# Kernel optimization log

Hardware: AMD Instinct MI355X
Metric: run time of the kernel (lower is better)

## Reference

```python
import jax, jax.numpy as jnp
import numpy as np

H = 1024
L = 2

def setup_inputs() -> dict:
    key = jax.random.key(0)
    k1, k2, k3, k4, k5 = jax.random.split(key, 5)
    B, S = 32, 2048
    scale = 1.0 / np.sqrt(H)
    return {
        "query": jax.random.normal(k1, (B, 1, H * L), dtype=jnp.float32),
        "keys": jax.random.normal(k2, (B, S, H), dtype=jnp.float32),
        "Wa_w": jax.random.normal(k3, (H * L, H), dtype=jnp.float32) * scale,
        "Wa_b": jnp.zeros((H,), dtype=jnp.float32),
        "Ua_w": jax.random.normal(k4, (H, H), dtype=jnp.float32) * scale,
        "Ua_b": jnp.zeros((H,), dtype=jnp.float32),
        "Va_w": jax.random.normal(k5, (H, 1), dtype=jnp.float32) * scale,
        "Va_b": jnp.zeros((1,), dtype=jnp.float32),
    }

def reference(query, keys, Wa_w, Wa_b, Ua_w, Ua_b, Va_w, Va_b):
    # query: [B,1,H*L], keys: [B,S,H]
    q = jnp.einsum('bqd,dh->bqh', query, Wa_w) + Wa_b   # [B,1,H]
    k = jnp.einsum('bsd,dh->bsh', keys, Ua_w) + Ua_b    # [B,S,H]
    e = jnp.tanh(q + k)                                  # [B,S,H]
    scores = jnp.einsum('bsh,ho->bso', e, Va_w) + Va_b   # [B,S,1]
    scores = scores[:, :, 0][:, None, :]                 # [B,1,S]
    weights = jax.nn.softmax(scores, axis=-1)            # [B,1,S]
    context = jnp.einsum('bqs,bsh->bqh', weights, keys)  # [B,1,H]
    return (context, weights)
```

## Files before the change

kernel.cpp:

```cpp
#include <hip/hip_runtime.h>
#include <hip/hip_bf16.h>


typedef __attribute__((ext_vector_type(8))) short short8;
typedef __attribute__((ext_vector_type(4))) float floatx4;

typedef const __attribute__((address_space(1))) unsigned int gu32;
typedef __attribute__((address_space(3))) unsigned int lu32;

__device__ __forceinline__ unsigned short f2bf(float f) {
    union { float f; unsigned int u; } c; c.f = f;
    unsigned int u = c.u + 0x7fffu + ((c.u >> 16) & 1u);
    return (unsigned short)(u >> 16);
}

__device__ __forceinline__ unsigned int f2bf2(float lo, float hi) {
#if __has_builtin(__builtin_amdgcn_cvt_pk_bf16_f32)
    auto r = __builtin_amdgcn_cvt_pk_bf16_f32(lo, hi);
    unsigned int u; __builtin_memcpy(&u, &r, 4);
    return u;
#else
    return (unsigned int)f2bf(lo) | ((unsigned int)f2bf(hi) << 16);
#endif
}

__device__ __forceinline__ void gld16(const unsigned short* g, unsigned short* l) {
    __builtin_amdgcn_global_load_lds(
        (gu32*)(uintptr_t)g,
        (lu32*)(unsigned int)(uintptr_t)l,
        16, 0, 0);
}

__global__ __launch_bounds__(256) void qproj_k(
    const float* __restrict__ query, const float* __restrict__ Wa,
    const float* __restrict__ Wab, const float* __restrict__ Uab,
    float* __restrict__ qws)
{
    __shared__ float qs[2048];
    __shared__ float red[16*64];
    const int tid = threadIdx.x;
    const int b = blockIdx.x, hc = blockIdx.y;
    #pragma unroll
    for (int i = 0; i < 8; i++) qs[tid + 256*i] = query[b*2048 + tid + 256*i];
    __syncthreads();
    const int hq = tid & 15;
    const int dg = tid >> 4;
    const float4* wp = reinterpret_cast<const float4*>(Wa + (size_t)(dg*128)*1024 + hc*64 + hq*4);
    const float* qp = qs + dg*128;
    float4 a0; a0.x = a0.y = a0.z = a0.w = 0.f;
    float4 a1; a1.x = a1.y = a1.z = a1.w = 0.f;
    #pragma unroll 4
    for (int d = 0; d < 128; d += 2) {
        float q0 = qp[d], q1 = qp[d+1];
        float4 w0 = wp[(size_t)d*256];
        float4 w1 = wp[(size_t)(d+1)*256];
        a0.x += q0*w0.x; a0.y += q0*w0.y; a0.z += q0*w0.z; a0.w += q0*w0.w;
        a1.x += q1*w1.x; a1.y += q1*w1.y; a1.z += q1*w1.z; a1.w += q1*w1.w;
    }
    a0.x += a1.x; a0.y += a1.y; a0.z += a1.z; a0.w += a1.w;
    *reinterpret_cast<float4*>(red + dg*64 + hq*4) = a0;
    __syncthreads();
    if (tid < 64) {
        float v = 0.f;
        #pragma unroll
        for (int g = 0; g < 16; g++) v += red[g*64 + tid];
        int hh = hc*64 + tid;
        qws[b*1024 + hh] = v + Wab[hh] + Uab[hh];
    }
}

__global__ __launch_bounds__(256) void uat_k(const float* __restrict__ Ua,
                                             unsigned short* __restrict__ uat)
{
    __shared__ unsigned short t[64][65];
    const int x = threadIdx.x & 63, yy = threadIdx.x >> 6;
    const int d0 = blockIdx.x*64, h0 = blockIdx.y*64;
    #pragma unroll
    for (int i = 0; i < 16; i++) {
        int y = yy*16 + i;
        t[y][x] = f2bf(Ua[(size_t)(d0+y)*1024 + h0 + x]);
    }
    __syncthreads();
    #pragma unroll
    for (int i = 0; i < 16; i++) {
        int y = yy*16 + i;
        uat[(size_t)(h0+y)*1024 + d0 + x] = t[x][y];
    }
}

__global__ __launch_bounds__(256) void score_gemm_fast(
    const float* __restrict__ keys,
    const unsigned short* __restrict__ uat,
    const float* __restrict__ qws,
    const float* __restrict__ Va,
    float* __restrict__ partial)
{
    __shared__ unsigned short aS[2][128*32];
    __shared__ unsigned short bS[2][128*32];
    const int tid = threadIdx.x;
    const int b = blockIdx.z;
    const int s0 = blockIdx.x * 128;
    const int h0 = blockIdx.y * 128;
    const int lane = tid & 63, wave = tid >> 6;
    const int quad = lane >> 4, l15 = lane & 15;
    const int wm = (wave & 1) * 64, wn = (wave >> 1) * 64;

    const int srow = lane >> 2;
    const int schunk = (lane & 3) ^ ((srow >> 1) & 3);

    floatx4 acc[4][4];
    #pragma unroll
    for (int i = 0; i < 4; i++)
        #pragma unroll
        for (int j = 0; j < 4; j++) acc[i][j] = (floatx4)0.0f;

    const float* kA = keys + (size_t)(b*2048 + s0)*1024;
    const unsigned short* ubase = uat + (size_t)h0*1024;
    const int c0 = wave*2, c1 = wave*2 + 1;
    const size_t boff0 = (size_t)(c0*16 + srow)*1024 + schunk*8;
    const size_t boff1 = (size_t)(c1*16 + srow)*1024 + schunk*8;

    const int arow0 = tid >> 2, ac = tid & 3;

    gld16(ubase + boff0, bS[0] + c0*512);
    gld16(ubase + boff1, bS[0] + c1*512);
    #pragma unroll
    for (int i = 0; i < 2; i++) {
        int row = arow0 + 64*i;
        int sl  = ac ^ ((row >> 1) & 3);
        const float* gp = kA + (size_t)row*1024 + ac*8;
        float4 v0 = *reinterpret_cast<const float4*>(gp);
        float4 v1 = *reinterpret_cast<const float4*>(gp + 4);
        uint4 w;
        w.x = f2bf2(v0.x, v0.y); w.y = f2bf2(v0.z, v0.w);
        w.z = f2bf2(v1.x, v1.y); w.w = f2bf2(v1.z, v1.w);
        *reinterpret_cast<uint4*>(aS[0] + row*32 + sl*8) = w;
    }
    __syncthreads();

    int cur = 0;
    for (int kt = 0; kt < 31; ++kt) {
        const int nxt = cur ^ 1;
        const int k1 = (kt + 1) << 5;

        gld16(ubase + boff0 + k1, bS[nxt] + c0*512);
        gld16(ubase + boff1 + k1, bS[nxt] + c1*512);
        float4 pa0[2], pa1[2];
        #pragma unroll
        for (int i = 0; i < 2; i++) {
            int row = arow0 + 64*i;
            const float* gp = kA + (size_t)row*1024 + k1 + ac*8;
            pa0[i] = *reinterpret_cast<const float4*>(gp);
            pa1[i] = *reinterpret_cast<const float4*>(gp + 4);
        }

        short8 af[4], bf8[4];
        #pragma unroll
        for (int i = 0; i < 4; i++) {
            int row = wm + 16*i + l15;
            af[i] = *reinterpret_cast<const short8*>(aS[cur] + row*32 + ((quad ^ ((row>>1)&3)) * 8));
        }
        #pragma unroll
        for (int j = 0; j < 4; j++) {
            int row = wn + 16*j + l15;
            bf8[j] = *reinterpret_cast<const short8*>(bS[cur] + row*32 + ((quad ^ ((row>>1)&3)) * 8));
        }
        __builtin_amdgcn_s_setprio(1);
        #pragma unroll
        for (int i = 0; i < 4; i++)
            #pragma unroll
            for (int j = 0; j < 4; j++)
                acc[i][j] = __builtin_amdgcn_mfma_f32_16x16x32_bf16(af[i], bf8[j], acc[i][j], 0, 0, 0);
        __builtin_amdgcn_s_setprio(0);

        #pragma unroll
        for (int i = 0; i < 2; i++) {
            int row = arow0 + 64*i;
            int sl  = ac ^ ((row >> 1) & 3);
            uint4 w;
            w.x = f2bf2(pa0[i].x, pa0[i].y); w.y = f2bf2(pa0[i].z, pa0[i].w);
            w.z = f2bf2(pa1[i].x, pa1[i].y); w.w = f2bf2(pa1[i].z, pa1[i].w);
            *reinterpret_cast<uint4*>(aS[nxt] + row*32 + sl*8) = w;
        }
        __syncthreads();
        cur = nxt;
    }

    {
        short8 af[4], bf8[4];
        #pragma unroll
        for (int i = 0; i < 4; i++) {
            int row = wm + 16*i + l15;
            af[i] = *reinterpret_cast<const short8*>(aS[cur] + row*32 + ((quad ^ ((row>>1)&3)) * 8));
        }
        #pragma unroll
        for (int j = 0; j < 4; j++) {
            int row = wn + 16*j + l15;
            bf8[j] = *reinterpret_cast<const short8*>(bS[cur] + row*32 + ((quad ^ ((row>>1)&3)) * 8));
        }
        __builtin_amdgcn_s_setprio(1);
        #pragma unroll
        for (int i = 0; i < 4; i++)
            #pragma unroll
            for (int j = 0; j < 4; j++)
                acc[i][j] = __builtin_amdgcn_mfma_f32_16x16x32_bf16(af[i], bf8[j], acc[i][j], 0, 0, 0);
        __builtin_amdgcn_s_setprio(0);
    }

    float qv[4], vav[4];
    #pragma unroll
    for (int j = 0; j < 4; j++) {
        int n = h0 + wn + 16*j + l15;
        qv[j]  = qws[b*1024 + n];
        vav[j] = Va[n];
    }
    const int slot = blockIdx.y * 2 + (wave >> 1);
    #pragma unroll
    for (int i = 0; i < 4; i++) {
        #pragma unroll
        for (int r = 0; r < 4; r++) {
            float p = 0.f;
            #pragma unroll
            for (int j = 0; j < 4; j++) {
                float x = qv[j] + acc[i][j][r];
                float e = __expf(2.f * x);
                float t = 1.f - 2.f * __builtin_amdgcn_rcpf(e + 1.f);
                p += vav[j] * t;
            }
            #pragma unroll
            for (int off = 1; off < 16; off <<= 1) p += __shfl_xor(p, off, 64);
            if (l15 == 0) {
                int m = wm + 16*i + quad*4 + r;
                partial[((size_t)b*16 + slot)*2048 + s0 + m] = p;
            }
        }
    }
}

__global__ __launch_bounds__(256) void softmax_k(const float* __restrict__ partial,
                                                 float* __restrict__ out_w)
{
    const int tid = threadIdx.x;
    const int b = blockIdx.x;
    __shared__ float wred[4], wred2[4];
    float sc[8];
    float mx = -3.0e38f;
    #pragma unroll
    for (int i = 0; i < 8; i++) {
        int s = tid + 256*i;
        float v = 0.f;
        #pragma unroll
        for (int ht = 0; ht < 16; ht++) v += partial[((size_t)b*16 + ht)*2048 + s];
        sc[i] = v; mx = fmaxf(mx, v);
    }
    #pragma unroll
    for (int off = 32; off >= 1; off >>= 1) mx = fmaxf(mx, __shfl_xor(mx, off, 64));
    if ((tid & 63) == 0) wred[tid >> 6] = mx;
    __syncthreads();
    mx = fmaxf(fmaxf(wred[0], wred[1]), fmaxf(wred[2], wred[3]));
    float e[8]; float lsum = 0.f;
    #pragma unroll
    for (int i = 0; i < 8; i++) { e[i] = __expf(sc[i] - mx); lsum += e[i]; }
    #pragma unroll
    for (int off = 32; off >= 1; off >>= 1) lsum += __shfl_xor(lsum, off, 64);
    if ((tid & 63) == 0) wred2[tid >> 6] = lsum;
    __syncthreads();
    float inv = 1.0f / (wred2[0] + wred2[1] + wred2[2] + wred2[3]);
    #pragma unroll
    for (int i = 0; i < 8; i++) out_w[b*2048 + tid + 256*i] = e[i] * inv;
}

__global__ __launch_bounds__(256) void ctx_k(const float* __restrict__ keys,
                                             const float* __restrict__ w,
                                             float* __restrict__ ctxp, int sper)
{
    const int tid = threadIdx.x;
    const int b = blockIdx.x, sc = blockIdx.y;
    const float4* k4 = reinterpret_cast<const float4*>(keys) + (size_t)(b*2048 + sc*sper)*256;
    const float* wp = w + b*2048 + sc*sper;
    float4 a; a.x = a.y = a.z = a.w = 0.f;
    #pragma unroll 4
    for (int s = 0; s < sper; s++) {
        float wv = wp[s];
        float4 kv = k4[(size_t)s*256 + tid];
        a.x += wv*kv.x; a.y += wv*kv.y; a.z += wv*kv.z; a.w += wv*kv.w;
    }
    reinterpret_cast<float4*>(ctxp)[((size_t)b*gridDim.y + sc)*256 + tid] = a;
}

__global__ __launch_bounds__(256) void ctxsum_k(const float* __restrict__ ctxp,
                                                float* __restrict__ out, int nc)
{
    const int idx = blockIdx.x*256 + threadIdx.x;
    const int b = idx >> 10, h = idx & 1023;
    float v = 0.f;
    for (int s = 0; s < nc; s++) v += ctxp[((size_t)b*nc + s)*1024 + h];
    out[idx] = v;
}

extern "C" void kernel_launch(void* const* d_in, const int* in_sizes, int n_in,
                              void* d_out, int out_size, void* d_ws, size_t ws_size,
                              hipStream_t stream)
{
    const float* query = (const float*)d_in[0];
    const float* keys  = (const float*)d_in[1];
    const float* Wa_w  = (const float*)d_in[2];
    const float* Wa_b  = (const float*)d_in[3];
    const float* Ua_w  = (const float*)d_in[4];
    const float* Ua_b  = (const float*)d_in[5];
    const float* Va_w  = (const float*)d_in[6];

    char* ws = (char*)d_ws;
    float*          qws     = (float*)(ws);
    unsigned short* uat     = (unsigned short*)(ws + (131072));
    float*          partial = (float*)(ws + (131072 + 2097152));
    float*          ctxp    = (float*)(ws + (131072 + 2097152 + 4194304));

    float* out_ctx = (float*)d_out;
    float* out_w   = out_ctx + 32*1024;

    qproj_k        <<<dim3(32, 16),    256, 0, stream>>>(query, Wa_w, Wa_b, Ua_b, qws);
    uat_k          <<<dim3(16, 16),    256, 0, stream>>>(Ua_w, uat);
    score_gemm_fast<<<dim3(16, 8, 32), 256, 0, stream>>>(keys, uat, qws, Va_w, partial);
    softmax_k      <<<dim3(32),        256, 0, stream>>>(partial, out_w);
    ctx_k          <<<dim3(32, 16),    256, 0, stream>>>(keys, out_w, ctxp, 128);
    ctxsum_k       <<<dim3(128),       256, 0, stream>>>(ctxp, out_ctx, 16);
}
```

Measured before the change: 665.7 us.

## Pre-convert keys to swizzled bf16 buffer and load GEMM A-tiles directly to LDS

Result: slower. 725.5 us (+9.0%).

```diff
diff --git a/kernel.cpp b/kernel.cpp
--- a/kernel.cpp
+++ b/kernel.cpp
@@ -88,17 +88,44 @@
     }
 }
 
+__global__ __launch_bounds__(256) void kb16_k(const float* __restrict__ keys,
+                                              unsigned short* __restrict__ kb)
+{
+    const size_t t = (size_t)blockIdx.x*256 + threadIdx.x;
+    const size_t rg = t >> 5;
+    const int g = (int)(t & 31);
+    const int s = (int)(rg & 2047);
+    const int p = (s >> 1) & 3;
+    const float4* in4 = reinterpret_cast<const float4*>(keys + rg*1024 + g*32);
+    uint4* out4 = reinterpret_cast<uint4*>(kb + rg*1024 + g*32);
+    float4 v[8];
+    #pragma unroll
+    for (int q = 0; q < 8; q++) v[q] = in4[q];
+    #pragma unroll
+    for (int j = 0; j < 4; j++) {
+        int jc = j ^ p;
+        uint4 w;
+        w.x = f2bf2(v[2*jc].x,   v[2*jc].y);
+        w.y = f2bf2(v[2*jc].z,   v[2*jc].w);
+        w.z = f2bf2(v[2*jc+1].x, v[2*jc+1].y);
+        w.w = f2bf2(v[2*jc+1].z, v[2*jc+1].w);
+        out4[j] = w;
+    }
+}
+
 __global__ __launch_bounds__(256) void score_gemm_fast(
-    const float* __restrict__ keys,
+    const unsigned short* __restrict__ kb16,
     const unsigned short* __restrict__ uat,
     const float* __restrict__ qws,
     const float* __restrict__ Va,
-    float* __restrict__ partial)
+    float* __restrict__ partial,
+    int b0)
 {
     __shared__ unsigned short aS[2][128*32];
     __shared__ unsigned short bS[2][128*32];
     const int tid = threadIdx.x;
-    const int b = blockIdx.z;
+    const int bz = blockIdx.z;
+    const int b = b0 + bz;
     const int s0 = blockIdx.x * 128;
     const int h0 = blockIdx.y * 128;
     const int lane = tid & 63, wave = tid >> 6;
@@ -107,35 +134,25 @@
 
     const int srow = lane >> 2;
     const int schunk = (lane & 3) ^ ((srow >> 1) & 3);
-
-    floatx4 acc[4][4];
-    #pragma unroll
-    for (int i = 0; i < 4; i++)
-        #pragma unroll
-        for (int j = 0; j < 4; j++) acc[i][j] = (floatx4)0.0f;
-
-    const float* kA = keys + (size_t)(b*2048 + s0)*1024;
+    const int c0 = wave*2, c1 = wave*2 + 1;
     const unsigned short* ubase = uat + (size_t)h0*1024;
-    const int c0 = wave*2, c1 = wave*2 + 1;
     const size_t boff0 = (size_t)(c0*16 + srow)*1024 + schunk*8;
     const size_t boff1 = (size_t)(c1*16 + srow)*1024 + schunk*8;
 
-    const int arow0 = tid >> 2, ac = tid & 3;
-
+    const unsigned short* kA = kb16 + (size_t)(bz*2048 + s0)*1024;
+    const size_t aoff0 = (size_t)(tid >> 2)*1024 + (size_t)(tid & 3)*8;
+    const size_t aoff1 = (size_t)(64 + (tid >> 2))*1024 + (size_t)(tid & 3)*8;
+
+    floatx4 acc[4][4];
+    #pragma unroll
+    for (int i = 0; i < 4; i++)
+        #pragma unroll
+        for (int j = 0; j < 4; j++) acc[i][j] = (floatx4)0.0f;
+
+    gld16(kA + aoff0,    aS[0] + wave*512);
+    gld16(kA + aoff1,    aS[0] + 2048 + wave*512);
     gld16(ubase + boff0, bS[0] + c0*512);
     gld16(ubase + boff1, bS[0] + c1*512);
-    #pragma unroll
-    for (int i = 0; i < 2; i++) {
-        int row = arow0 + 64*i;
-        int sl  = ac ^ ((row >> 1) & 3);
-        const float* gp = kA + (size_t)row*1024 + ac*8;
-        float4 v0 = *reinterpret_cast<const float4*>(gp);
-        float4 v1 = *reinterpret_cast<const float4*>(gp + 4);
-        uint4 w;
-        w.x = f2bf2(v0.x, v0.y); w.y = f2bf2(v0.z, v0.w);
-        w.z = f2bf2(v1.x, v1.y); w.w = f2bf2(v1.z, v1.w);
-        *reinterpret_cast<uint4*>(aS[0] + row*32 + sl*8) = w;
-    }
     __syncthreads();
 
     int cur = 0;
@@ -143,16 +160,10 @@
         const int nxt = cur ^ 1;
         const int k1 = (kt + 1) << 5;
 
+        gld16(kA + aoff0 + k1,    aS[nxt] + wave*512);
+        gld16(kA + aoff1 + k1,    aS[nxt] + 2048 + wave*512);
         gld16(ubase + boff0 + k1, bS[nxt] + c0*512);
         gld16(ubase + boff1 + k1, bS[nxt] + c1*512);
-        float4 pa0[2], pa1[2];
-        #pragma unroll
-        for (int i = 0; i < 2; i++) {
-            int row = arow0 + 64*i;
-            const float* gp = kA + (size_t)row*1024 + k1 + ac*8;
-            pa0[i] = *reinterpret_cast<const float4*>(gp);
-            pa1[i] = *reinterpret_cast<const float4*>(gp + 4);
-        }
 
         short8 af[4], bf8[4];
         #pragma unroll
@@ -165,23 +176,12 @@
             int row = wn + 16*j + l15;
             bf8[j] = *reinterpret_cast<const short8*>(bS[cur] + row*32 + ((quad ^ ((row>>1)&3)) * 8));
         }
-        __builtin_amdgcn_s_setprio(1);
         #pragma unroll
         for (int i = 0; i < 4; i++)
             #pragma unroll
             for (int j = 0; j < 4; j++)
                 acc[i][j] = __builtin_amdgcn_mfma_f32_16x16x32_bf16(af[i], bf8[j], acc[i][j], 0, 0, 0);
-        __builtin_amdgcn_s_setprio(0);
-
-        #pragma unroll
-        for (int i = 0; i < 2; i++) {
-            int row = arow0 + 64*i;
-            int sl  = ac ^ ((row >> 1) & 3);
-            uint4 w;
-            w.x = f2bf2(pa0[i].x, pa0[i].y); w.y = f2bf2(pa0[i].z, pa0[i].w);
-            w.z = f2bf2(pa1[i].x, pa1[i].y); w.w = f2bf2(pa1[i].z, pa1[i].w);
-            *reinterpret_cast<uint4*>(aS[nxt] + row*32 + sl*8) = w;
-        }
+
         __syncthreads();
         cur = nxt;
     }
@@ -198,13 +198,11 @@
             int row = wn + 16*j + l15;
             bf8[j] = *reinterpret_cast<const short8*>(bS[cur] + row*32 + ((quad ^ ((row>>1)&3)) * 8));
         }
-        __builtin_amdgcn_s_setprio(1);
         #pragma unroll
         for (int i = 0; i < 4; i++)
             #pragma unroll
             for (int j = 0; j < 4; j++)
                 acc[i][j] = __builtin_amdgcn_mfma_f32_16x16x32_bf16(af[i], bf8[j], acc[i][j], 0, 0, 0);
-        __builtin_amdgcn_s_setprio(0);
     }
 
     float qv[4], vav[4];
@@ -315,14 +313,23 @@
     unsigned short* uat     = (unsigned short*)(ws + (131072));
     float*          partial = (float*)(ws + (131072 + 2097152));
     float*          ctxp    = (float*)(ws + (131072 + 2097152 + 4194304));
+    const size_t BASE = 131072 + 2097152 + 4194304 + 2097152;
+    unsigned short* kb16 = (unsigned short*)(ws + BASE);
+
+    size_t avail = (ws_size > BASE) ? (ws_size - BASE) : 0;
+    int nb = 32;
+    while (nb > 1 && (size_t)nb * 2048 * 1024 * 2 > avail) nb >>= 1;
 
     float* out_ctx = (float*)d_out;
     float* out_w   = out_ctx + 32*1024;
 
-    qproj_k        <<<dim3(32, 16),    256, 0, stream>>>(query, Wa_w, Wa_b, Ua_b, qws);
-    uat_k          <<<dim3(16, 16),    256, 0, stream>>>(Ua_w, uat);
-    score_gemm_fast<<<dim3(16, 8, 32), 256, 0, stream>>>(keys, uat, qws, Va_w, partial);
-    softmax_k      <<<dim3(32),        256, 0, stream>>>(partial, out_w);
-    ctx_k          <<<dim3(32, 16),    256, 0, stream>>>(keys, out_w, ctxp, 128);
-    ctxsum_k       <<<dim3(128),       256, 0, stream>>>(ctxp, out_ctx, 16);
-}
+    qproj_k<<<dim3(32, 16), 256, 0, stream>>>(query, Wa_w, Wa_b, Ua_b, qws);
+    uat_k  <<<dim3(16, 16), 256, 0, stream>>>(Ua_w, uat);
+    for (int b0 = 0; b0 < 32; b0 += nb) {
+        kb16_k<<<dim3(nb*256), 256, 0, stream>>>(keys + (size_t)b0*2048*1024, kb16);
+        score_gemm_fast<<<dim3(16, 8, nb), 256, 0, stream>>>(kb16, uat, qws, Va_w, partial, b0);
+    }
+    softmax_k<<<dim3(32),      256, 0, stream>>>(partial, out_w);
+    ctx_k    <<<dim3(32, 16),  256, 0, stream>>>(keys, out_w, ctxp, 128);
+    ctxsum_k <<<dim3(128),     256, 0, stream>>>(ctxp, out_ctx, 16);
+}
```
